# Optimization experiments

Measured on AMD Instinct MI355X. Metric: run time of the kernel, lower is better.

The kernel has to match this reference:

```python
import jax, jax.numpy as jnp
import numpy as np

B, N, C = 32, 16384, 256
D, H, S = 64, 128, 7
ITERS = 3
EPS = 1e-6
SCALE = D ** -0.5


def _ln(x, g, b):
    m = jnp.mean(x, axis=-1, keepdims=True)
    v = jnp.var(x, axis=-1, keepdims=True)
    return (x - m) / jnp.sqrt(v + 1e-5) * g + b


def _gru(x, h, Wih, Whh, bih, bhh):
    # PyTorch GRUCell: Wih/Whh are [3D, D]
    gi = x @ Wih.T + bih
    gh = h @ Whh.T + bhh
    ir, iz, inn = jnp.split(gi, 3, axis=-1)
    hr, hz, hn = jnp.split(gh, 3, axis=-1)
    r = jax.nn.sigmoid(ir + hr)
    z = jax.nn.sigmoid(iz + hz)
    n = jnp.tanh(inn + r * hn)
    return (1.0 - z) * n + z * h


def setup_inputs() -> dict:
    key = jax.random.key(0)
    ks = jax.random.split(key, 20)
    s_c = C ** -0.5
    s_d = D ** -0.5
    s_h = H ** -0.5
    p = {}
    p["inputs"] = jax.random.normal(ks[0], (B, N, C), jnp.float32)
    p["slots_mu"] = jax.random.normal(ks[1], (B, S, D), jnp.float32)
    p["ln_in_g"] = jnp.ones((C,), jnp.float32)
    p["ln_in_b"] = jnp.zeros((C,), jnp.float32)
    p["Wk"] = jax.random.normal(ks[2], (C, D), jnp.float32) * s_c
    p["Wv"] = jax.random.normal(ks[3], (C, D), jnp.float32) * s_c
    p["q_ln_g"] = jnp.ones((D,), jnp.float32)
    p["q_ln_b"] = jnp.zeros((D,), jnp.float32)
    p["Wq"] = jax.random.normal(ks[4], (D, D), jnp.float32) * s_d
    p["bq_ln_g"] = jnp.ones((D,), jnp.float32)
    p["bq_ln_b"] = jnp.zeros((D,), jnp.float32)
    p["bWq"] = jax.random.normal(ks[5], (D, D), jnp.float32) * s_d
    p["gru_Wih"] = jax.random.normal(ks[6], (3 * D, D), jnp.float32) * s_d
    p["gru_Whh"] = jax.random.normal(ks[7], (3 * D, D), jnp.float32) * s_d
    p["gru_bih"] = jnp.zeros((3 * D,), jnp.float32)
    p["gru_bhh"] = jnp.zeros((3 * D,), jnp.float32)
    p["mlp_ln_g"] = jnp.ones((D,), jnp.float32)
    p["mlp_ln_b"] = jnp.zeros((D,), jnp.float32)
    p["mlp_W1"] = jax.random.normal(ks[8], (D, H), jnp.float32) * s_d
    p["mlp_b1"] = jnp.zeros((H,), jnp.float32)
    p["mlp_W2"] = jax.random.normal(ks[9], (H, D), jnp.float32) * s_h
    p["mlp_b2"] = jnp.zeros((D,), jnp.float32)
    p["bmlp_ln_g"] = jnp.ones((D,), jnp.float32)
    p["bmlp_ln_b"] = jnp.zeros((D,), jnp.float32)
    p["bmlp_W1"] = jax.random.normal(ks[10], (D, H), jnp.float32) * s_d
    p["bmlp_b1"] = jnp.zeros((H,), jnp.float32)
    p["bmlp_W2"] = jax.random.normal(ks[11], (H, D), jnp.float32) * s_h
    p["bmlp_b2"] = jnp.zeros((D,), jnp.float32)
    return p


def reference(inputs, slots_mu, ln_in_g, ln_in_b, Wk, Wv, q_ln_g, q_ln_b, Wq,
              bq_ln_g, bq_ln_b, bWq, gru_Wih, gru_Whh, gru_bih, gru_bhh,
              mlp_ln_g, mlp_ln_b, mlp_W1, mlp_b1, mlp_W2, mlp_b2,
              bmlp_ln_g, bmlp_ln_b, bmlp_W1, bmlp_b1, bmlp_W2, bmlp_b2):
    x = _ln(inputs, ln_in_g, ln_in_b)          # [B,N,C]
    k = x @ Wk                                  # [B,N,D]
    v = x @ Wv                                  # [B,N,D]
    fg = slots_mu[:, :-1]                       # [B,S-1,D]
    bg = slots_mu[:, -1:]                       # [B,1,D]
    for _ in range(ITERS):
        fg_prev, bg_prev = fg, bg
        fq = _ln(fg, q_ln_g, q_ln_b) @ Wq
        bq = _ln(bg, bq_ln_g, bq_ln_b) @ bWq
        q = jnp.concatenate([fq, bq], axis=1)   # [B,S,D]
        logits = SCALE * jnp.einsum('bnd,bmd->bnm', k, q)  # [B,N,S]
        attn = jax.nn.softmax(logits, axis=-1) + EPS
        fa = attn[..., :-1]
        ba = attn[..., -1:]
        fa = fa / jnp.sum(fa, axis=1, keepdims=True)
        ba = ba / jnp.sum(ba, axis=1, keepdims=True)
        fu = jnp.einsum('bnm,bnd->bmd', fa, v)  # [B,S-1,D]
        bu = jnp.einsum('bnm,bnd->bmd', ba, v)  # [B,1,D]
        fg = _gru(fu.reshape(-1, D), fg_prev.reshape(-1, D),
                  gru_Wih, gru_Whh, gru_bih, gru_bhh).reshape(B, S - 1, D)
        fg = fg + (jax.nn.relu(_ln(fg, mlp_ln_g, mlp_ln_b) @ mlp_W1 + mlp_b1) @ mlp_W2 + mlp_b2)
        # NOTE: original code uses self.gru (shared) for bg, not bg_gru
        bg = _gru(bu.reshape(-1, D), bg_prev.reshape(-1, D),
                  gru_Wih, gru_Whh, gru_bih, gru_bhh).reshape(B, 1, D)
        bg = bg + (jax.nn.relu(_ln(bg, bmlp_ln_g, bmlp_ln_b) @ bmlp_W1 + bmlp_b1) @ bmlp_W2 + bmlp_b2)
    return jnp.concatenate([fg, bg], axis=1)    # [B,S,D]
```

## Files before the change

### kernel.cpp

```cpp
#include <hip/hip_runtime.h>
#include <hip/hip_bf16.h>

typedef __bf16 bf16_t;
typedef __bf16 bf16x4 __attribute__((ext_vector_type(4)));
typedef __bf16 bf16x8 __attribute__((ext_vector_type(8)));
typedef float f32x4 __attribute__((ext_vector_type(4)));

#define B_ 32
#define N_ 16384
#define C_ 256
#define D_ 64
#define ROWS_TOTAL (B_ * N_)

__device__ inline float wave_sum64(float v) {
#pragma unroll
  for (int o = 1; o < 64; o <<= 1) v += __shfl_xor(v, o);
  return v;
}

__device__ inline float sigmoidf_(float x) { return 1.0f / (1.0f + __expf(-x)); }
__device__ inline float tanhf_(float x) { return 1.0f - 2.0f / (__expf(2.0f * x) + 1.0f); }

__global__ __launch_bounds__(256) void prep_kernel(
    const float* __restrict__ Wk, const float* __restrict__ Wv,
    const float* __restrict__ Wih, const float* __restrict__ Whh,
    const float* __restrict__ slots, bf16_t* __restrict__ Wb,
    float* __restrict__ WihT, float* __restrict__ WhhT, float* __restrict__ g) {
  int i = blockIdx.x * 256 + threadIdx.x;
  if (i < 32768) {
    int j = i & 7, l = (i >> 3) & 63, t = (i >> 9) & 7, kb = i >> 12;
    int k = kb * 32 + (l >> 4) * 8 + j;
    int n = t * 16 + (l & 15);
    float v = (n < 64) ? Wk[k * 64 + n] : Wv[k * 64 + (n - 64)];
    Wb[i] = (bf16_t)v;
  } else if (i < 45056) {
    int idx = i - 32768;
    int c = idx / 192, j = idx % 192;
    WihT[idx] = Wih[j * 64 + c];
  } else if (i < 57344) {
    int idx = i - 45056;
    int c = idx / 192, j = idx % 192;
    WhhT[idx] = Whh[j * 64 + c];
  } else if (i < 71680) {
    int idx = i - 57344;
    g[idx] = slots[idx];
  }
}

__global__ __launch_bounds__(256) void proj_ln_kernel(
    const float* __restrict__ inp, const float* __restrict__ lng,
    const float* __restrict__ lnb, const bf16_t* __restrict__ Wb,
    bf16_t* __restrict__ kbuf, bf16_t* __restrict__ vbuf) {
  __shared__ bf16_t xs[128 * 256];
  const int tid = threadIdx.x, w = tid >> 6, lane = tid & 63;
  const int q4 = lane >> 4, lp = lane & 15;
  const long row0 = (long)blockIdx.x * 128;

  float4 gv = *(const float4*)(lng + lane * 4);
  float4 bv = *(const float4*)(lnb + lane * 4);

  for (int i = 0; i < 32; ++i) {
    int r = w * 32 + i;
    float4 x = *(const float4*)(inp + (row0 + r) * C_ + lane * 4);
    float s = x.x + x.y + x.z + x.w;
    float s2 = x.x * x.x + x.y * x.y + x.z * x.z + x.w * x.w;
#pragma unroll
    for (int o = 1; o < 64; o <<= 1) {
      s += __shfl_xor(s, o);
      s2 += __shfl_xor(s2, o);
    }
    float mean = s * (1.0f / 256.0f);
    float var = s2 * (1.0f / 256.0f) - mean * mean;
    float rstd = rsqrtf(var + 1e-5f);
    bf16x4 y;
    y[0] = (bf16_t)((x.x - mean) * rstd * gv.x + bv.x);
    y[1] = (bf16_t)((x.y - mean) * rstd * gv.y + bv.y);
    y[2] = (bf16_t)((x.z - mean) * rstd * gv.z + bv.z);
    y[3] = (bf16_t)((x.w - mean) * rstd * gv.w + bv.w);
    size_t unit = (size_t)(r * 32 + ((lane >> 1) ^ (r & 31)));
    *(bf16x4*)(xs + unit * 8 + (lane & 1) * 4) = y;
  }
  __syncthreads();

  f32x4 acc[2][8];
  const f32x4 zf = {0.0f, 0.0f, 0.0f, 0.0f};
#pragma unroll
  for (int mt = 0; mt < 2; ++mt)
#pragma unroll
    for (int t = 0; t < 8; ++t) acc[mt][t] = zf;

  for (int kb = 0; kb < 8; ++kb) {
    int cidx = kb * 4 + q4;
    int r0 = w * 32 + lp;
    int r1 = r0 + 16;
    bf16x8 a0 = *(const bf16x8*)(xs + (size_t)(r0 * 32 + (cidx ^ (r0 & 31))) * 8);
    bf16x8 a1 = *(const bf16x8*)(xs + (size_t)(r1 * 32 + (cidx ^ (r1 & 31))) * 8);
#pragma unroll
    for (int t = 0; t < 8; ++t) {
      bf16x8 bf = *(const bf16x8*)(Wb + (size_t)((kb * 8 + t) * 64 + lane) * 8);
      acc[0][t] = __builtin_amdgcn_mfma_f32_16x16x32_bf16(a0, bf, acc[0][t], 0, 0, 0);
      acc[1][t] = __builtin_amdgcn_mfma_f32_16x16x32_bf16(a1, bf, acc[1][t], 0, 0, 0);
    }
  }

#pragma unroll
  for (int mt = 0; mt < 2; ++mt) {
#pragma unroll
    for (int t = 0; t < 8; ++t) {
      bf16_t* dst = (t < 4) ? kbuf : vbuf;
      int c = (t & 3) * 16 + lp;
#pragma unroll
      for (int reg = 0; reg < 4; ++reg) {
        long gr = row0 + w * 32 + mt * 16 + q4 * 4 + reg;
        dst[gr * 64 + c] = (bf16_t)acc[mt][t][reg];
      }
    }
  }
}

__global__ __launch_bounds__(64) void qk_kernel(
    const float* __restrict__ g, const float* __restrict__ qg,
    const float* __restrict__ qb, const float* __restrict__ Wq,
    const float* __restrict__ bqg, const float* __restrict__ bqb,
    const float* __restrict__ bWq, float* __restrict__ q,
    float* __restrict__ acc, float* __restrict__ wsum) {
  __shared__ float sx[64];
  int bid = blockIdx.x, lane = threadIdx.x;
  int m = bid % 7;
  const float* lng = (m < 6) ? qg : bqg;
  const float* lnb = (m < 6) ? qb : bqb;
  const float* W = (m < 6) ? Wq : bWq;
  float gv = g[bid * 64 + lane];
  float s = wave_sum64(gv);
  float s2 = wave_sum64(gv * gv);
  float mean = s * (1.0f / 64.0f);
  float var = s2 * (1.0f / 64.0f) - mean * mean;
  float rstd = rsqrtf(var + 1e-5f);
  sx[lane] = (gv - mean) * rstd * lng[lane] + lnb[lane];
  __syncthreads();
  float qd = 0.0f;
#pragma unroll 8
  for (int c = 0; c < 64; ++c) qd += sx[c] * W[c * 64 + lane];
  q[bid * 64 + lane] = qd;
  acc[bid * 64 + lane] = 0.0f;
  if (lane == 0) wsum[bid] = 0.0f;
}

__global__ __launch_bounds__(256) void attend_kernel(
    const bf16_t* __restrict__ kbuf, const bf16_t* __restrict__ vbuf,
    const float* __restrict__ q, float* __restrict__ acc,
    float* __restrict__ wsum) {
  __shared__ float qs[448];
  __shared__ float s_acc[448];
  __shared__ float s_w[7];
  int tid = threadIdx.x, w = tid >> 6, lane = tid & 63;
  int g4 = lane >> 4, lp = lane & 15;
  long chunk0 = (long)blockIdx.x * 512;
  int b = (int)(chunk0 >> 14);

  for (int idx = tid; idx < 448; idx += 256) {
    qs[idx] = q[b * 448 + idx];
    s_acc[idx] = 0.0f;
  }
  if (tid < 7) s_w[tid] = 0.0f;
  __syncthreads();

  float av[7][4];
  float wa[7];
#pragma unroll
  for (int m = 0; m < 7; ++m) {
    wa[m] = 0.0f;
#pragma unroll
    for (int j = 0; j < 4; ++j) av[m][j] = 0.0f;
  }

  const float4* qs4 = (const float4*)qs;
  for (int it = 0; it < 32; ++it) {
    long row = chunk0 + it * 16 + w * 4 + g4;
    bf16x4 kv = *(const bf16x4*)(kbuf + row * 64 + lp * 4);
    bf16x4 vv = *(const bf16x4*)(vbuf + row * 64 + lp * 4);
    float k0 = kv[0], k1 = kv[1], k2 = kv[2], k3 = kv[3];
    float lg[7];
#pragma unroll
    for (int m = 0; m < 7; ++m) {
      float4 qv = qs4[m * 16 + lp];
      lg[m] = k0 * qv.x + k1 * qv.y + k2 * qv.z + k3 * qv.w;
    }
#pragma unroll
    for (int m = 0; m < 7; ++m) {
      lg[m] += __shfl_xor(lg[m], 1);
      lg[m] += __shfl_xor(lg[m], 2);
      lg[m] += __shfl_xor(lg[m], 4);
      lg[m] += __shfl_xor(lg[m], 8);
    }
    float mx = -1e30f;
#pragma unroll
    for (int m = 0; m < 7; ++m) {
      lg[m] *= 0.125f;
      mx = fmaxf(mx, lg[m]);
    }
    float e[7], s = 0.0f;
#pragma unroll
    for (int m = 0; m < 7; ++m) {
      e[m] = __expf(lg[m] - mx);
      s += e[m];
    }
    float inv = 1.0f / s;
    float v0 = vv[0], v1 = vv[1], v2 = vv[2], v3 = vv[3];
#pragma unroll
    for (int m = 0; m < 7; ++m) {
      float a = e[m] * inv + 1e-6f;
      wa[m] += a;
      av[m][0] += a * v0;
      av[m][1] += a * v1;
      av[m][2] += a * v2;
      av[m][3] += a * v3;
    }
  }

#pragma unroll
  for (int m = 0; m < 7; ++m) {
#pragma unroll
    for (int j = 0; j < 4; ++j) {
      av[m][j] += __shfl_xor(av[m][j], 16);
      av[m][j] += __shfl_xor(av[m][j], 32);
    }
    wa[m] += __shfl_xor(wa[m], 16);
    wa[m] += __shfl_xor(wa[m], 32);
  }
  if (g4 == 0) {
#pragma unroll
    for (int m = 0; m < 7; ++m)
#pragma unroll
      for (int j = 0; j < 4; ++j) atomicAdd(&s_acc[m * 64 + lp * 4 + j], av[m][j]);
  }
  if (lane == 0) {
#pragma unroll
    for (int m = 0; m < 7; ++m) atomicAdd(&s_w[m], wa[m]);
  }
  __syncthreads();
  for (int idx = tid; idx < 448; idx += 256) atomicAdd(&acc[b * 448 + idx], s_acc[idx]);
  if (tid < 7) atomicAdd(&wsum[b * 7 + tid], s_w[tid]);
}

__global__ __launch_bounds__(192) void update_kernel(
    const float* __restrict__ acc, const float* __restrict__ wsum,
    const float* __restrict__ g, const float* __restrict__ WihT,
    const float* __restrict__ WhhT, const float* __restrict__ bih,
    const float* __restrict__ bhh, const float* __restrict__ mlg,
    const float* __restrict__ mlb, const float* __restrict__ mW1,
    const float* __restrict__ mb1, const float* __restrict__ mW2,
    const float* __restrict__ mb2, const float* __restrict__ bmlg,
    const float* __restrict__ bmlb, const float* __restrict__ bW1,
    const float* __restrict__ bb1, const float* __restrict__ bW2,
    const float* __restrict__ bb2, float* __restrict__ gout) {
  __shared__ float fu[64], hp[64], gi[192], gh[192], h2[64], xb[64], a1[128];
  int tid = threadIdx.x, bid = blockIdx.x, m = bid % 7;

  const float* lg_;
  const float* lb_;
  const float* W1_;
  const float* b1_;
  const float* W2_;
  const float* b2_;
  if (m < 6) { lg_ = mlg; lb_ = mlb; W1_ = mW1; b1_ = mb1; W2_ = mW2; b2_ = mb2; }
  else       { lg_ = bmlg; lb_ = bmlb; W1_ = bW1; b1_ = bb1; W2_ = bW2; b2_ = bb2; }

  if (tid < 64) {
    float wv = wsum[bid];
    fu[tid] = acc[bid * 64 + tid] / wv;
    hp[tid] = g[bid * 64 + tid];
  }
  __syncthreads();

  {
    int j = tid;
    float a = bih[j], bsum = bhh[j];
    for (int c = 0; c < 64; ++c) {
      a += fu[c] * WihT[c * 192 + j];
      bsum += hp[c] * WhhT[c * 192 + j];
    }
    gi[j] = a;
    gh[j] = bsum;
  }
  __syncthreads();

  if (tid < 64) {
    int d = tid;
    float r = sigmoidf_(gi[d] + gh[d]);
    float z = sigmoidf_(gi[64 + d] + gh[64 + d]);
    float n = tanhf_(gi[128 + d] + r * gh[128 + d]);
    float h = (1.0f - z) * n + z * hp[d];
    h2[d] = h;
    float s = wave_sum64(h);
    float s2 = wave_sum64(h * h);
    float mean = s * (1.0f / 64.0f);
    float var = s2 * (1.0f / 64.0f) - mean * mean;
    xb[d] = (h - mean) * rsqrtf(var + 1e-5f) * lg_[d] + lb_[d];
  }
  __syncthreads();

  if (tid < 128) {
    int hh = tid;
    float a = b1_[hh];
    for (int c = 0; c < 64; ++c) a += xb[c] * W1_[c * 128 + hh];
    a1[hh] = fmaxf(a, 0.0f);
  }
  __syncthreads();

  if (tid < 64) {
    int d = tid;
    float o = b2_[d];
    for (int hh = 0; hh < 128; ++hh) o += a1[hh] * W2_[hh * 64 + d];
    gout[bid * 64 + d] = h2[d] + o;
  }
}

extern "C" void kernel_launch(void* const* d_in, const int* in_sizes, int n_in,
                              void* d_out, int out_size, void* d_ws, size_t ws_size,
                              hipStream_t stream) {
  const float* inputs   = (const float*)d_in[0];
  const float* slots_mu = (const float*)d_in[1];
  const float* ln_in_g  = (const float*)d_in[2];
  const float* ln_in_b  = (const float*)d_in[3];
  const float* Wk       = (const float*)d_in[4];
  const float* Wv       = (const float*)d_in[5];
  const float* q_ln_g   = (const float*)d_in[6];
  const float* q_ln_b   = (const float*)d_in[7];
  const float* Wq       = (const float*)d_in[8];
  const float* bq_ln_g  = (const float*)d_in[9];
  const float* bq_ln_b  = (const float*)d_in[10];
  const float* bWq      = (const float*)d_in[11];
  const float* gru_Wih  = (const float*)d_in[12];
  const float* gru_Whh  = (const float*)d_in[13];
  const float* gru_bih  = (const float*)d_in[14];
  const float* gru_bhh  = (const float*)d_in[15];
  const float* mlp_ln_g = (const float*)d_in[16];
  const float* mlp_ln_b = (const float*)d_in[17];
  const float* mlp_W1   = (const float*)d_in[18];
  const float* mlp_b1   = (const float*)d_in[19];
  const float* mlp_W2   = (const float*)d_in[20];
  const float* mlp_b2   = (const float*)d_in[21];
  const float* bmlp_ln_g = (const float*)d_in[22];
  const float* bmlp_ln_b = (const float*)d_in[23];
  const float* bmlp_W1  = (const float*)d_in[24];
  const float* bmlp_b1  = (const float*)d_in[25];
  const float* bmlp_W2  = (const float*)d_in[26];
  const float* bmlp_b2  = (const float*)d_in[27];
  float* out = (float*)d_out;

  char* ws = (char*)d_ws;
  const size_t KV_BYTES = (size_t)ROWS_TOTAL * 64 * 2;
  bf16_t* kbuf = (bf16_t*)ws;
  bf16_t* vbuf = (bf16_t*)(ws + KV_BYTES);
  bf16_t* Wb   = (bf16_t*)(ws + 2 * KV_BYTES);
  float* WihT  = (float*)(ws + 2 * KV_BYTES + 65536);
  float* WhhT  = (float*)(ws + 2 * KV_BYTES + 65536 + 49152);
  float* gbuf  = (float*)(ws + 2 * KV_BYTES + 65536 + 2 * 49152);
  float* qbuf  = (float*)(ws + 2 * KV_BYTES + 65536 + 2 * 49152 + 57344);
  float* accb  = (float*)(ws + 2 * KV_BYTES + 65536 + 2 * 49152 + 2 * 57344);
  float* wsumb = (float*)(ws + 2 * KV_BYTES + 65536 + 2 * 49152 + 3 * 57344);

  prep_kernel<<<280, 256, 0, stream>>>(Wk, Wv, gru_Wih, gru_Whh, slots_mu, Wb,
                                       WihT, WhhT, gbuf);
  proj_ln_kernel<<<ROWS_TOTAL / 128, 256, 0, stream>>>(inputs, ln_in_g, ln_in_b,
                                                       Wb, kbuf, vbuf);
  for (int it = 0; it < 3; ++it) {
    qk_kernel<<<224, 64, 0, stream>>>(gbuf, q_ln_g, q_ln_b, Wq, bq_ln_g, bq_ln_b,
                                      bWq, qbuf, accb, wsumb);
    attend_kernel<<<ROWS_TOTAL / 512, 256, 0, stream>>>(kbuf, vbuf, qbuf, accb,
                                                        wsumb);
    update_kernel<<<224, 192, 0, stream>>>(
        accb, wsumb, gbuf, WihT, WhhT, gru_bih, gru_bhh, mlp_ln_g, mlp_ln_b,
        mlp_W1, mlp_b1, mlp_W2, mlp_b2, bmlp_ln_g, bmlp_ln_b, bmlp_W1, bmlp_b1,
        bmlp_W2, bmlp_b2, (it == 2) ? out : gbuf);
  }
}
```

Before: 1.054 ms.

## Restructure LN-projection to 512 threads, hoist q into registers, fuse q into update

The LayerNorm+projection kernel now runs 8 waves of 16 rows each, with 16 lanes per row doing 16-element vector loads and a 16-lane reduction, halving per-wave accumulators. The attend kernel hoists the per-slot query vectors from shared memory into registers once, outside the row loop. The q computation and accumulator zeroing for the next iteration are fused into the tail of the update kernel, removing two qk launches. The risks are extra register pressure and a __syncwarp inside a block-divergent branch.

```diff
diff --git a/kernel.cpp b/kernel.cpp
--- a/kernel.cpp
+++ b/kernel.cpp
@@ -47,7 +47,7 @@
   }
 }
 
-__global__ __launch_bounds__(256) void proj_ln_kernel(
+__global__ __launch_bounds__(512) void proj_ln_kernel(
     const float* __restrict__ inp, const float* __restrict__ lng,
     const float* __restrict__ lnb, const bf16_t* __restrict__ Wb,
     bf16_t* __restrict__ kbuf, bf16_t* __restrict__ vbuf) {
@@ -56,64 +56,82 @@
   const int q4 = lane >> 4, lp = lane & 15;
   const long row0 = (long)blockIdx.x * 128;
 
-  float4 gv = *(const float4*)(lng + lane * 4);
-  float4 bv = *(const float4*)(lnb + lane * 4);
-
-  for (int i = 0; i < 32; ++i) {
-    int r = w * 32 + i;
-    float4 x = *(const float4*)(inp + (row0 + r) * C_ + lane * 4);
-    float s = x.x + x.y + x.z + x.w;
-    float s2 = x.x * x.x + x.y * x.y + x.z * x.z + x.w * x.w;
-#pragma unroll
-    for (int o = 1; o < 64; o <<= 1) {
+  float4 gv[4], bv[4];
+#pragma unroll
+  for (int j = 0; j < 4; ++j) {
+    gv[j] = *(const float4*)(lng + lp * 16 + j * 4);
+    bv[j] = *(const float4*)(lnb + lp * 16 + j * 4);
+  }
+
+#pragma unroll
+  for (int i = 0; i < 4; ++i) {
+    int r = w * 16 + i * 4 + q4;
+    const float* rp = inp + (row0 + r) * C_ + lp * 16;
+    float4 x0 = *(const float4*)(rp);
+    float4 x1 = *(const float4*)(rp + 4);
+    float4 x2 = *(const float4*)(rp + 8);
+    float4 x3 = *(const float4*)(rp + 12);
+    float s = (x0.x + x0.y + x0.z + x0.w) + (x1.x + x1.y + x1.z + x1.w) +
+              (x2.x + x2.y + x2.z + x2.w) + (x3.x + x3.y + x3.z + x3.w);
+    float s2 = (x0.x * x0.x + x0.y * x0.y + x0.z * x0.z + x0.w * x0.w) +
+               (x1.x * x1.x + x1.y * x1.y + x1.z * x1.z + x1.w * x1.w) +
+               (x2.x * x2.x + x2.y * x2.y + x2.z * x2.z + x2.w * x2.w) +
+               (x3.x * x3.x + x3.y * x3.y + x3.z * x3.z + x3.w * x3.w);
+#pragma unroll
+    for (int o = 1; o < 16; o <<= 1) {
       s += __shfl_xor(s, o);
       s2 += __shfl_xor(s2, o);
     }
     float mean = s * (1.0f / 256.0f);
     float var = s2 * (1.0f / 256.0f) - mean * mean;
     float rstd = rsqrtf(var + 1e-5f);
-    bf16x4 y;
-    y[0] = (bf16_t)((x.x - mean) * rstd * gv.x + bv.x);
-    y[1] = (bf16_t)((x.y - mean) * rstd * gv.y + bv.y);
-    y[2] = (bf16_t)((x.z - mean) * rstd * gv.z + bv.z);
-    y[3] = (bf16_t)((x.w - mean) * rstd * gv.w + bv.w);
-    size_t unit = (size_t)(r * 32 + ((lane >> 1) ^ (r & 31)));
-    *(bf16x4*)(xs + unit * 8 + (lane & 1) * 4) = y;
-  }
-  __syncthreads();
-
-  f32x4 acc[2][8];
+    bf16x8 y0, y1;
+    y0[0] = (bf16_t)((x0.x - mean) * rstd * gv[0].x + bv[0].x);
+    y0[1] = (bf16_t)((x0.y - mean) * rstd * gv[0].y + bv[0].y);
+    y0[2] = (bf16_t)((x0.z - mean) * rstd * gv[0].z + bv[0].z);
+    y0[3] = (bf16_t)((x0.w - mean) * rstd * gv[0].w + bv[0].w);
+    y0[4] = (bf16_t)((x1.x - mean) * rstd * gv[1].x + bv[1].x);
+    y0[5] = (bf16_t)((x1.y - mean) * rstd * gv[1].y + bv[1].y);
+    y0[6] = (bf16_t)((x1.z - mean) * rstd * gv[1].z + bv[1].z);
+    y0[7] = (bf16_t)((x1.w - mean) * rstd * gv[1].w + bv[1].w);
+    y1[0] = (bf16_t)((x2.x - mean) * rstd * gv[2].x + bv[2].x);
+    y1[1] = (bf16_t)((x2.y - mean) * rstd * gv[2].y + bv[2].y);
+    y1[2] = (bf16_t)((x2.z - mean) * rstd * gv[2].z + bv[2].z);
+    y1[3] = (bf16_t)((x2.w - mean) * rstd * gv[2].w + bv[2].w);
+    y1[4] = (bf16_t)((x3.x - mean) * rstd * gv[3].x + bv[3].x);
+    y1[5] = (bf16_t)((x3.y - mean) * rstd * gv[3].y + bv[3].y);
+    y1[6] = (bf16_t)((x3.z - mean) * rstd * gv[3].z + bv[3].z);
+    y1[7] = (bf16_t)((x3.w - mean) * rstd * gv[3].w + bv[3].w);
+    int base = r * 32, swz = r & 31;
+    *(bf16x8*)(xs + (size_t)(base + ((2 * lp) ^ swz)) * 8) = y0;
+    *(bf16x8*)(xs + (size_t)(base + ((2 * lp + 1) ^ swz)) * 8) = y1;
+  }
+  __syncthreads();
+
+  f32x4 acc[8];
   const f32x4 zf = {0.0f, 0.0f, 0.0f, 0.0f};
 #pragma unroll
-  for (int mt = 0; mt < 2; ++mt)
-#pragma unroll
-    for (int t = 0; t < 8; ++t) acc[mt][t] = zf;
-
+  for (int t = 0; t < 8; ++t) acc[t] = zf;
+
+  const int r0 = w * 16 + lp;
+  const int rsw = r0 & 31;
   for (int kb = 0; kb < 8; ++kb) {
-    int cidx = kb * 4 + q4;
-    int r0 = w * 32 + lp;
-    int r1 = r0 + 16;
-    bf16x8 a0 = *(const bf16x8*)(xs + (size_t)(r0 * 32 + (cidx ^ (r0 & 31))) * 8);
-    bf16x8 a1 = *(const bf16x8*)(xs + (size_t)(r1 * 32 + (cidx ^ (r1 & 31))) * 8);
+    bf16x8 a = *(const bf16x8*)(xs + (size_t)(r0 * 32 + ((kb * 4 + q4) ^ rsw)) * 8);
 #pragma unroll
     for (int t = 0; t < 8; ++t) {
-      bf16x8 bf = *(const bf16x8*)(Wb + (size_t)((kb * 8 + t) * 64 + lane) * 8);
-      acc[0][t] = __builtin_amdgcn_mfma_f32_16x16x32_bf16(a0, bf, acc[0][t], 0, 0, 0);
-      acc[1][t] = __builtin_amdgcn_mfma_f32_16x16x32_bf16(a1, bf, acc[1][t], 0, 0, 0);
-    }
-  }
-
-#pragma unroll
-  for (int mt = 0; mt < 2; ++mt) {
-#pragma unroll
-    for (int t = 0; t < 8; ++t) {
-      bf16_t* dst = (t < 4) ? kbuf : vbuf;
-      int c = (t & 3) * 16 + lp;
-#pragma unroll
-      for (int reg = 0; reg < 4; ++reg) {
-        long gr = row0 + w * 32 + mt * 16 + q4 * 4 + reg;
-        dst[gr * 64 + c] = (bf16_t)acc[mt][t][reg];
-      }
+      bf16x8 bfr = *(const bf16x8*)(Wb + (size_t)((kb * 8 + t) * 64 + lane) * 8);
+      acc[t] = __builtin_amdgcn_mfma_f32_16x16x32_bf16(a, bfr, acc[t], 0, 0, 0);
+    }
+  }
+
+#pragma unroll
+  for (int t = 0; t < 8; ++t) {
+    bf16_t* dst = (t < 4) ? kbuf : vbuf;
+    int c = (t & 3) * 16 + lp;
+#pragma unroll
+    for (int reg = 0; reg < 4; ++reg) {
+      long gr = row0 + w * 16 + q4 * 4 + reg;
+      dst[gr * 64 + c] = (bf16_t)acc[t][reg];
     }
   }
 }
@@ -130,13 +148,13 @@
   const float* lng = (m < 6) ? qg : bqg;
   const float* lnb = (m < 6) ? qb : bqb;
   const float* W = (m < 6) ? Wq : bWq;
-  float gv = g[bid * 64 + lane];
-  float s = wave_sum64(gv);
-  float s2 = wave_sum64(gv * gv);
+  float gvv = g[bid * 64 + lane];
+  float s = wave_sum64(gvv);
+  float s2 = wave_sum64(gvv * gvv);
   float mean = s * (1.0f / 64.0f);
   float var = s2 * (1.0f / 64.0f) - mean * mean;
   float rstd = rsqrtf(var + 1e-5f);
-  sx[lane] = (gv - mean) * rstd * lng[lane] + lnb[lane];
+  sx[lane] = (gvv - mean) * rstd * lng[lane] + lnb[lane];
   __syncthreads();
   float qd = 0.0f;
 #pragma unroll 8
@@ -165,6 +183,11 @@
   if (tid < 7) s_w[tid] = 0.0f;
   __syncthreads();
 
+  float4 qv[7];
+  const float4* qs4 = (const float4*)qs;
+#pragma unroll
+  for (int m = 0; m < 7; ++m) qv[m] = qs4[m * 16 + lp];
+
   float av[7][4];
   float wa[7];
 #pragma unroll
@@ -174,7 +197,6 @@
     for (int j = 0; j < 4; ++j) av[m][j] = 0.0f;
   }
 
-  const float4* qs4 = (const float4*)qs;
   for (int it = 0; it < 32; ++it) {
     long row = chunk0 + it * 16 + w * 4 + g4;
     bf16x4 kv = *(const bf16x4*)(kbuf + row * 64 + lp * 4);
@@ -182,10 +204,8 @@
     float k0 = kv[0], k1 = kv[1], k2 = kv[2], k3 = kv[3];
     float lg[7];
 #pragma unroll
-    for (int m = 0; m < 7; ++m) {
-      float4 qv = qs4[m * 16 + lp];
-      lg[m] = k0 * qv.x + k1 * qv.y + k2 * qv.z + k3 * qv.w;
-    }
+    for (int m = 0; m < 7; ++m)
+      lg[m] = k0 * qv[m].x + k1 * qv[m].y + k2 * qv[m].z + k3 * qv[m].w;
 #pragma unroll
     for (int m = 0; m < 7; ++m) {
       lg[m] += __shfl_xor(lg[m], 1);
@@ -253,16 +273,16 @@
     const float* __restrict__ mb2, const float* __restrict__ bmlg,
     const float* __restrict__ bmlb, const float* __restrict__ bW1,
     const float* __restrict__ bb1, const float* __restrict__ bW2,
-    const float* __restrict__ bb2, float* __restrict__ gout) {
-  __shared__ float fu[64], hp[64], gi[192], gh[192], h2[64], xb[64], a1[128];
+    const float* __restrict__ bb2, float* __restrict__ gout,
+    const float* __restrict__ qg, const float* __restrict__ qb,
+    const float* __restrict__ Wq, const float* __restrict__ bqg,
+    const float* __restrict__ bqb, const float* __restrict__ bWq,
+    float* __restrict__ qout, float* __restrict__ accz,
+    float* __restrict__ wsz, int write_q) {
+  __shared__ float fu[64], hp[64], gi[192], gh[192], h2[64], xb[64], a1[128], go[64];
   int tid = threadIdx.x, bid = blockIdx.x, m = bid % 7;
 
-  const float* lg_;
-  const float* lb_;
-  const float* W1_;
-  const float* b1_;
-  const float* W2_;
-  const float* b2_;
+  const float *lg_, *lb_, *W1_, *b1_, *W2_, *b2_;
   if (m < 6) { lg_ = mlg; lb_ = mlb; W1_ = mW1; b1_ = mb1; W2_ = mW2; b2_ = mb2; }
   else       { lg_ = bmlg; lb_ = bmlb; W1_ = bW1; b1_ = bb1; W2_ = bW2; b2_ = bb2; }
 
@@ -312,7 +332,32 @@
     int d = tid;
     float o = b2_[d];
     for (int hh = 0; hh < 128; ++hh) o += a1[hh] * W2_[hh * 64 + d];
-    gout[bid * 64 + d] = h2[d] + o;
+    float res = h2[d] + o;
+    gout[bid * 64 + d] = res;
+    go[d] = res;
+  }
+  __syncthreads();
+
+  if (write_q) {
+    if (tid < 64) {
+      const float* qlng = (m < 6) ? qg : bqg;
+      const float* qlnb = (m < 6) ? qb : bqb;
+      const float* W = (m < 6) ? Wq : bWq;
+      float gvv = go[tid];
+      float s = wave_sum64(gvv);
+      float s2 = wave_sum64(gvv * gvv);
+      float mean = s * (1.0f / 64.0f);
+      float var = s2 * (1.0f / 64.0f) - mean * mean;
+      xb[tid] = (gvv - mean) * rsqrtf(var + 1e-5f) * qlng[tid] + qlnb[tid];
+      __syncwarp();
+      float qd = 0.0f;
+      const float* Wl = W;
+#pragma unroll 8
+      for (int c = 0; c < 64; ++c) qd += xb[c] * Wl[c * 64 + tid];
+      qout[bid * 64 + tid] = qd;
+      accz[bid * 64 + tid] = 0.0f;
+      if (tid == 0) wsz[bid] = 0.0f;
+    }
   }
 }
 
@@ -363,16 +408,17 @@
 
   prep_kernel<<<280, 256, 0, stream>>>(Wk, Wv, gru_Wih, gru_Whh, slots_mu, Wb,
                                        WihT, WhhT, gbuf);
-  proj_ln_kernel<<<ROWS_TOTAL / 128, 256, 0, stream>>>(inputs, ln_in_g, ln_in_b,
+  proj_ln_kernel<<<ROWS_TOTAL / 128, 512, 0, stream>>>(inputs, ln_in_g, ln_in_b,
                                                        Wb, kbuf, vbuf);
+  qk_kernel<<<224, 64, 0, stream>>>(gbuf, q_ln_g, q_ln_b, Wq, bq_ln_g, bq_ln_b,
+                                    bWq, qbuf, accb, wsumb);
   for (int it = 0; it < 3; ++it) {
-    qk_kernel<<<224, 64, 0, stream>>>(gbuf, q_ln_g, q_ln_b, Wq, bq_ln_g, bq_ln_b,
-                                      bWq, qbuf, accb, wsumb);
     attend_kernel<<<ROWS_TOTAL / 512, 256, 0, stream>>>(kbuf, vbuf, qbuf, accb,
                                                         wsumb);
     update_kernel<<<224, 192, 0, stream>>>(
         accb, wsumb, gbuf, WihT, WhhT, gru_bih, gru_bhh, mlp_ln_g, mlp_ln_b,
         mlp_W1, mlp_b1, mlp_W2, mlp_b2, bmlp_ln_g, bmlp_ln_b, bmlp_W1, bmlp_b1,
-        bmlp_W2, bmlp_b2, (it == 2) ? out : gbuf);
-  }
-}
+        bmlp_W2, bmlp_b2, (it == 2) ? out : gbuf, q_ln_g, q_ln_b, Wq, bq_ln_g,
+        bq_ln_b, bWq, qbuf, accb, wsumb, (it < 2) ? 1 : 0);
+  }
+}
```

New measurement: 1.036 ms. About the same (-1.7%).
